# Kernel optimization log

Hardware: AMD Instinct MI355X
Metric: run time of the kernel (lower is better)

The kernel has to match this reference:

```python
import jax, jax.numpy as jnp
import numpy as np

B, T, C, H = 4, 2048, 1024, 16
D = C // H
NEG = -1e9


def setup_inputs() -> dict:
    key = jax.random.key(0)
    ks = jax.random.split(key, 4)
    x = jax.random.normal(ks[0], (B, T, C), dtype=jnp.float32)
    # additive causal mask: 0 on/below diagonal, -1e9 above
    causal = jnp.triu(jnp.full((T, T), NEG, dtype=jnp.float32), k=1)
    mask = causal[None, None, :, :]
    W_attn = jax.random.normal(ks[1], (C, 3 * C), dtype=jnp.float32) * (1.0 / np.sqrt(C))
    b_attn = jnp.zeros((3 * C,), dtype=jnp.float32)
    W_proj = jax.random.normal(ks[2], (C, C), dtype=jnp.float32) * (1.0 / np.sqrt(C))
    b_proj = jnp.zeros((C,), dtype=jnp.float32)
    return {"x": x, "mask": mask, "W_attn": W_attn, "b_attn": b_attn,
            "W_proj": W_proj, "b_proj": b_proj}


def reference(x, mask, W_attn, b_attn, W_proj, b_proj):
    b, t, c = x.shape
    qkv = x @ W_attn + b_attn                      # [b,t,3c]
    q, k, v = jnp.split(qkv, 3, axis=2)
    # [b,h,t,d]
    q = q.reshape(b, t, H, D).transpose(0, 2, 1, 3)
    k = k.reshape(b, t, H, D).transpose(0, 2, 1, 3)
    v = v.reshape(b, t, H, D).transpose(0, 2, 1, 3)
    att = jnp.einsum('bhqd,bhkd->bhqk', q, k) * (1.0 / np.sqrt(D))
    att = att + mask
    att = jax.nn.softmax(att, axis=-1)
    out = jnp.einsum('bhqk,bhkd->bhqd', att, v)    # [b,h,t,d]
    out = out.transpose(0, 2, 1, 3).reshape(b, t, c)
    out = out @ W_proj + b_proj
    return out, k, v
```

## Files before the change

kernel.cpp:

```cpp
#include <hip/hip_runtime.h>
#include <stdint.h>

typedef short  s16x8 __attribute__((ext_vector_type(8)));
typedef ushort u16x8 __attribute__((ext_vector_type(8)));
typedef float  f32x4 __attribute__((ext_vector_type(4)));

constexpr int BB = 4, TT = 2048, CC = 1024, HH = 16, DD = 64;
constexpr int MM = BB * TT;
constexpr int N_QKV = 3 * CC;
constexpr size_t KSEG = (size_t)MM * CC;
constexpr size_t VSEG = 2 * KSEG;

__device__ __forceinline__ ushort bf16_rne(float f) {
  uint32_t u = __builtin_bit_cast(uint32_t, f);
  u += 0x7fffu + ((u >> 16) & 1u);
  return (ushort)(u >> 16);
}
__device__ __forceinline__ float bf16_to_f32(ushort h) {
  uint32_t u = ((uint32_t)h) << 16;
  return __builtin_bit_cast(float, u);
}
__device__ __forceinline__ void split_hl(float f, ushort &hi, ushort &lo) {
  hi = bf16_rne(f);
  lo = bf16_rne(f - bf16_to_f32(hi));
}
__device__ __forceinline__ f32x4 mfma16(s16x8 a, s16x8 b, f32x4 c) {
  return __builtin_amdgcn_mfma_f32_16x16x32_bf16(a, b, c, 0, 0, 0);
}

__global__ void k_convert(const float* __restrict__ src, ushort* __restrict__ hi,
                          ushort* __restrict__ lo, int n8) {
  int i = blockIdx.x * blockDim.x + threadIdx.x;
  if (i >= n8) return;
  float4 a = ((const float4*)src)[2 * i];
  float4 b = ((const float4*)src)[2 * i + 1];
  float f[8] = {a.x, a.y, a.z, a.w, b.x, b.y, b.z, b.w};
  u16x8 h, l;
#pragma unroll
  for (int j = 0; j < 8; j++) { ushort hh, ll; split_hl(f[j], hh, ll); h[j] = hh; l[j] = ll; }
  *(u16x8*)(hi + 8 * (size_t)i) = h;
  *(u16x8*)(lo + 8 * (size_t)i) = l;
}

__global__ void k_transpose_split(const float* __restrict__ W, ushort* __restrict__ Th,
                                  ushort* __restrict__ Tl, int K, int N) {
  __shared__ float tile[32][33];
  int nt = blockIdx.x * 32, kt = blockIdx.y * 32;
  int tx = threadIdx.x, ty = threadIdx.y;
#pragma unroll
  for (int i = 0; i < 4; i++)
    tile[ty + i * 8][tx] = W[(size_t)(kt + ty + i * 8) * N + nt + tx];
  __syncthreads();
#pragma unroll
  for (int i = 0; i < 4; i++) {
    int nl = ty + i * 8;
    float f = tile[tx][nl];
    ushort h, l; split_hl(f, h, l);
    size_t o = (size_t)(nt + nl) * K + kt + tx;
    Th[o] = h; Tl[o] = l;
  }
}

template<int MODE>
__global__ __launch_bounds__(256) void k_gemm(
    const ushort* __restrict__ Ah, const ushort* __restrict__ Al,
    const ushort* __restrict__ Bth, const ushort* __restrict__ Btl,
    const float* __restrict__ bias, int K,
    float* __restrict__ outF, ushort* __restrict__ q_hi, ushort* __restrict__ q_lo,
    ushort* __restrict__ kh, ushort* __restrict__ kl,
    ushort* __restrict__ vth, ushort* __restrict__ vtl) {
  constexpr int LDK = 40;
  __shared__ ushort sAh[128 * LDK], sAl[128 * LDK], sBh[128 * LDK], sBl[128 * LDK];
  const int tid = threadIdx.x;
  const int wave = tid >> 6, lane = tid & 63;
  const int wr = wave >> 1, wc = wave & 1;
  const int lr = lane & 15, lg = lane >> 4;
  const int m0 = blockIdx.y * 128, n0 = blockIdx.x * 128;
  const int srow = tid >> 2;
  const int sk = (tid & 3) * 8;

  f32x4 acc[4][4] = {};

  for (int kt = 0; kt < K; kt += 32) {
#pragma unroll
    for (int p = 0; p < 2; p++) {
      int row = srow + p * 64;
      size_t ga = (size_t)(m0 + row) * K + kt + sk;
      size_t gb = (size_t)(n0 + row) * K + kt + sk;
      *(u16x8*)(sAh + row * LDK + sk) = *(const u16x8*)(Ah + ga);
      *(u16x8*)(sAl + row * LDK + sk) = *(const u16x8*)(Al + ga);
      *(u16x8*)(sBh + row * LDK + sk) = *(const u16x8*)(Bth + gb);
      *(u16x8*)(sBl + row * LDK + sk) = *(const u16x8*)(Btl + gb);
    }
    __syncthreads();
    s16x8 fah[4], fal[4], fbh[4], fbl[4];
#pragma unroll
    for (int i = 0; i < 4; i++) {
      fah[i] = *(const s16x8*)(sAh + (wr * 64 + i * 16 + lr) * LDK + lg * 8);
      fal[i] = *(const s16x8*)(sAl + (wr * 64 + i * 16 + lr) * LDK + lg * 8);
      fbh[i] = *(const s16x8*)(sBh + (wc * 64 + i * 16 + lr) * LDK + lg * 8);
      fbl[i] = *(const s16x8*)(sBl + (wc * 64 + i * 16 + lr) * LDK + lg * 8);
    }
#pragma unroll
    for (int mf = 0; mf < 4; mf++)
#pragma unroll
      for (int nf = 0; nf < 4; nf++) {
        acc[mf][nf] = mfma16(fah[mf], fbh[nf], acc[mf][nf]);
        acc[mf][nf] = mfma16(fah[mf], fbl[nf], acc[mf][nf]);
        acc[mf][nf] = mfma16(fal[mf], fbh[nf], acc[mf][nf]);
      }
    __syncthreads();
  }

#pragma unroll
  for (int mf = 0; mf < 4; mf++) {
#pragma unroll
    for (int nf = 0; nf < 4; nf++) {
      int n = n0 + wc * 64 + nf * 16 + lr;
      float bv = bias[n];
#pragma unroll
      for (int r = 0; r < 4; r++) {
        int m = m0 + wr * 64 + mf * 16 + lg * 4 + r;
        float v = acc[mf][nf][r] + bv;
        if constexpr (MODE == 0) {
          int b = m >> 11, t = m & 2047;
          int seg = n >> 10, nn = n & 1023;
          int h = nn >> 6, d = nn & 63;
          size_t idx = ((size_t)((b * 16 + h) * 2048 + t)) * 64 + d;
          if (seg == 0) {
            ushort hh, ll; split_hl(v * 0.125f, hh, ll);
            q_hi[idx] = hh; q_lo[idx] = ll;
          } else if (seg == 1) {
            outF[KSEG + idx] = v;
            ushort hh, ll; split_hl(v, hh, ll);
            kh[idx] = hh; kl[idx] = ll;
          } else {
            outF[VSEG + idx] = v;
            ushort hh, ll; split_hl(v, hh, ll);
            size_t vidx = ((size_t)((b * 16 + h) * 64 + d)) * 2048 + t;
            vth[vidx] = hh; vtl[vidx] = ll;
          }
        } else {
          outF[(size_t)m * CC + n] = v;
        }
      }
    }
  }
}

__global__ __launch_bounds__(256) void k_attn(
    const ushort* __restrict__ q_hi, const ushort* __restrict__ q_lo,
    const ushort* __restrict__ kh, const ushort* __restrict__ kl,
    const ushort* __restrict__ vth, const ushort* __restrict__ vtl,
    ushort* __restrict__ att_hi, ushort* __restrict__ att_lo) {
  constexpr int LD = 72;
  __shared__ ushort sK0[64 * LD], sK1[64 * LD];
  __shared__ ushort sV0[64 * LD], sV1[64 * LD];
  const int tid = threadIdx.x, wave = tid >> 6, lane = tid & 63;
  const int lr = lane & 15, lg = lane >> 4;
  const int qt = blockIdx.x, bh = blockIdx.y;
  const int qrow = qt * 64 + wave * 16;

  s16x8 fqh[2], fql[2];
  {
    size_t qb = ((size_t)bh * TT + qrow + lr) * 64;
#pragma unroll
    for (int ks = 0; ks < 2; ks++) {
      fqh[ks] = *(const s16x8*)(q_hi + qb + ks * 32 + lg * 8);
      fql[ks] = *(const s16x8*)(q_lo + qb + ks * 32 + lg * 8);
    }
  }
  float mrun[4], lrun[4];
#pragma unroll
  for (int r = 0; r < 4; r++) { mrun[r] = -INFINITY; lrun[r] = 0.f; }
  f32x4 oacc[4] = {};

  ushort* const Pb0 = sK0 + wave * 16 * LD;
  ushort* const Pb1 = sK1 + wave * 16 * LD;

  for (int kt = 0; kt <= qt; kt++) {
#pragma unroll
    for (int it = 0; it < 2; it++) {
      int vv = tid + it * 256;
      int row = vv >> 3, c8 = (vv & 7) * 8;
      size_t gk = ((size_t)bh * TT + kt * 64 + row) * 64 + c8;
      size_t gv = ((size_t)bh * 64 + row) * TT + kt * 64 + c8;
      *(u16x8*)(sK0 + row * LD + c8) = *(const u16x8*)(kh + gk);
      *(u16x8*)(sK1 + row * LD + c8) = *(const u16x8*)(kl + gk);
      *(u16x8*)(sV0 + row * LD + c8) = *(const u16x8*)(vth + gv);
      *(u16x8*)(sV1 + row * LD + c8) = *(const u16x8*)(vtl + gv);
    }
    __syncthreads();

    f32x4 sa[4];
#pragma unroll
    for (int nf = 0; nf < 4; nf++) {
      f32x4 a = {};
#pragma unroll
      for (int ks = 0; ks < 2; ks++) {
        s16x8 kbh = *(const s16x8*)(sK0 + (nf * 16 + lr) * LD + ks * 32 + lg * 8);
        s16x8 kbl = *(const s16x8*)(sK1 + (nf * 16 + lr) * LD + ks * 32 + lg * 8);
        a = mfma16(fqh[ks], kbh, a);
        a = mfma16(fqh[ks], kbl, a);
        a = mfma16(fql[ks], kbh, a);
      }
      sa[nf] = a;
    }
    if (kt == qt) {
#pragma unroll
      for (int nf = 0; nf < 4; nf++) {
        int colg = qt * 64 + nf * 16 + lr;
#pragma unroll
        for (int r = 0; r < 4; r++)
          if (colg > qrow + 4 * lg + r) sa[nf][r] = -1e9f;
      }
    }
    float fr[4];
#pragma unroll
    for (int r = 0; r < 4; r++) {
      float mx = fmaxf(fmaxf(sa[0][r], sa[1][r]), fmaxf(sa[2][r], sa[3][r]));
      mx = fmaxf(mx, __shfl_xor(mx, 1));
      mx = fmaxf(mx, __shfl_xor(mx, 2));
      mx = fmaxf(mx, __shfl_xor(mx, 4));
      mx = fmaxf(mx, __shfl_xor(mx, 8));
      float mnew = fmaxf(mrun[r], mx);
      fr[r] = __expf(mrun[r] - mnew);
      mrun[r] = mnew;
    }
    __syncthreads();
    float rs[4] = {0.f, 0.f, 0.f, 0.f};
#pragma unroll
    for (int nf = 0; nf < 4; nf++) {
#pragma unroll
      for (int r = 0; r < 4; r++) {
        float p = __expf(sa[nf][r] - mrun[r]);
        rs[r] += p;
        ushort h, l; split_hl(p, h, l);
        Pb0[(4 * lg + r) * LD + nf * 16 + lr] = h;
        Pb1[(4 * lg + r) * LD + nf * 16 + lr] = l;
      }
    }
#pragma unroll
    for (int r = 0; r < 4; r++) {
      float s = rs[r];
      s += __shfl_xor(s, 1); s += __shfl_xor(s, 2);
      s += __shfl_xor(s, 4); s += __shfl_xor(s, 8);
      lrun[r] = lrun[r] * fr[r] + s;
    }
#pragma unroll
    for (int df = 0; df < 4; df++)
#pragma unroll
      for (int r = 0; r < 4; r++) oacc[df][r] *= fr[r];

#pragma unroll
    for (int ks = 0; ks < 2; ks++) {
      s16x8 ph = *(const s16x8*)(Pb0 + lr * LD + ks * 32 + lg * 8);
      s16x8 pl = *(const s16x8*)(Pb1 + lr * LD + ks * 32 + lg * 8);
#pragma unroll
      for (int df = 0; df < 4; df++) {
        s16x8 bvh = *(const s16x8*)(sV0 + (df * 16 + lr) * LD + ks * 32 + lg * 8);
        s16x8 bvl = *(const s16x8*)(sV1 + (df * 16 + lr) * LD + ks * 32 + lg * 8);
        oacc[df] = mfma16(ph, bvh, oacc[df]);
        oacc[df] = mfma16(ph, bvl, oacc[df]);
        oacc[df] = mfma16(pl, bvh, oacc[df]);
      }
    }
    __syncthreads();
  }

  const int b = bh >> 4, h = bh & 15;
#pragma unroll
  for (int r = 0; r < 4; r++) {
    float inv = 1.0f / lrun[r];
    int t = qrow + 4 * lg + r;
#pragma unroll
    for (int df = 0; df < 4; df++) {
      float v = oacc[df][r] * inv;
      ushort hh, ll; split_hl(v, hh, ll);
      size_t idx = ((size_t)(b * TT + t)) * CC + h * 64 + df * 16 + lr;
      att_hi[idx] = hh; att_lo[idx] = ll;
    }
  }
}

extern "C" void kernel_launch(void* const* d_in, const int* in_sizes, int n_in,
                              void* d_out, int out_size, void* d_ws, size_t ws_size,
                              hipStream_t stream) {
  const float* x      = (const float*)d_in[0];
  const float* W_attn = (const float*)d_in[2];
  const float* b_attn = (const float*)d_in[3];
  const float* W_proj = (const float*)d_in[4];
  const float* b_proj = (const float*)d_in[5];
  float* out = (float*)d_out;

  char* w = (char*)d_ws;
  ushort* x_hi  = (ushort*)w; w += (size_t)MM * CC * 2;
  ushort* x_lo  = (ushort*)w; w += (size_t)MM * CC * 2;
  ushort* waT_h = (ushort*)w; w += (size_t)N_QKV * CC * 2;
  ushort* waT_l = (ushort*)w; w += (size_t)N_QKV * CC * 2;
  ushort* wpT_h = (ushort*)w; w += (size_t)CC * CC * 2;
  ushort* wpT_l = (ushort*)w; w += (size_t)CC * CC * 2;
  ushort* q_hi  = (ushort*)w; w += (size_t)MM * CC * 2;
  ushort* q_lo  = (ushort*)w; w += (size_t)MM * CC * 2;
  ushort* k_hi  = (ushort*)w; w += (size_t)MM * CC * 2;
  ushort* k_lo  = (ushort*)w; w += (size_t)MM * CC * 2;
  ushort* vT_hi = (ushort*)w; w += (size_t)MM * CC * 2;
  ushort* vT_lo = (ushort*)w; w += (size_t)MM * CC * 2;
  ushort* att_h = x_hi;
  ushort* att_l = x_lo;

  hipLaunchKernelGGL(k_convert, dim3((MM * CC / 8 + 255) / 256), dim3(256), 0, stream,
                     x, x_hi, x_lo, MM * CC / 8);
  hipLaunchKernelGGL(k_transpose_split, dim3(N_QKV / 32, CC / 32), dim3(32, 8), 0, stream,
                     W_attn, waT_h, waT_l, CC, N_QKV);
  hipLaunchKernelGGL(k_transpose_split, dim3(CC / 32, CC / 32), dim3(32, 8), 0, stream,
                     W_proj, wpT_h, wpT_l, CC, CC);
  hipLaunchKernelGGL((k_gemm<0>), dim3(N_QKV / 128, MM / 128), dim3(256), 0, stream,
                     x_hi, x_lo, waT_h, waT_l, b_attn, CC, out, q_hi, q_lo,
                     k_hi, k_lo, vT_hi, vT_lo);
  hipLaunchKernelGGL(k_attn, dim3(TT / 64, BB * HH), dim3(256), 0, stream,
                     q_hi, q_lo, k_hi, k_lo, vT_hi, vT_lo, att_h, att_l);
  hipLaunchKernelGGL((k_gemm<1>), dim3(CC / 128, MM / 128), dim3(256), 0, stream,
                     att_h, att_l, wpT_h, wpT_l, b_proj, CC, out,
                     nullptr, nullptr, nullptr, nullptr, nullptr, nullptr);
}
```

Before: 850.4 us.

## Pair causal query tiles per block, swizzle LDS, lazily rescale softmax

The attention kernel now processes two query tiles per block (tile px and 31-px), so every block does the same amount of causal work and each K/V tile load serves both queries. LDS padding is replaced by an XOR swizzle in both the GEMM and attention kernels, cutting shared memory while avoiding bank conflicts. The online softmax skips rescaling unless the running max grows by more than 8. P gets its own LDS buffer so one barrier per step can be removed, and launch bounds request 3 blocks per CU. Holding two query tiles of accumulators raises register pressure, and the lazy rescale trades some numeric headroom in the exponentials.

```diff
diff --git a/kernel.cpp b/kernel.cpp
--- a/kernel.cpp
+++ b/kernel.cpp
@@ -10,6 +10,9 @@
 constexpr int N_QKV = 3 * CC;
 constexpr size_t KSEG = (size_t)MM * CC;
 constexpr size_t VSEG = 2 * KSEG;
+
+#define SWZ64(row, uoff) ((row) * 64 + ((uoff) ^ (((row) & 7) << 3)))
+#define SWZ32(row, uoff) ((row) * 32 + ((uoff) ^ (((row) & 3) << 3)))
 
 __device__ __forceinline__ ushort bf16_rne(float f) {
   uint32_t u = __builtin_bit_cast(uint32_t, f);
@@ -69,8 +72,7 @@
     float* __restrict__ outF, ushort* __restrict__ q_hi, ushort* __restrict__ q_lo,
     ushort* __restrict__ kh, ushort* __restrict__ kl,
     ushort* __restrict__ vth, ushort* __restrict__ vtl) {
-  constexpr int LDK = 40;
-  __shared__ ushort sAh[128 * LDK], sAl[128 * LDK], sBh[128 * LDK], sBl[128 * LDK];
+  __shared__ ushort sAh[128 * 32], sAl[128 * 32], sBh[128 * 32], sBl[128 * 32];
   const int tid = threadIdx.x;
   const int wave = tid >> 6, lane = tid & 63;
   const int wr = wave >> 1, wc = wave & 1;
@@ -87,19 +89,21 @@
       int row = srow + p * 64;
       size_t ga = (size_t)(m0 + row) * K + kt + sk;
       size_t gb = (size_t)(n0 + row) * K + kt + sk;
-      *(u16x8*)(sAh + row * LDK + sk) = *(const u16x8*)(Ah + ga);
-      *(u16x8*)(sAl + row * LDK + sk) = *(const u16x8*)(Al + ga);
-      *(u16x8*)(sBh + row * LDK + sk) = *(const u16x8*)(Bth + gb);
-      *(u16x8*)(sBl + row * LDK + sk) = *(const u16x8*)(Btl + gb);
+      int d = SWZ32(row, sk);
+      *(u16x8*)(sAh + d) = *(const u16x8*)(Ah + ga);
+      *(u16x8*)(sAl + d) = *(const u16x8*)(Al + ga);
+      *(u16x8*)(sBh + d) = *(const u16x8*)(Bth + gb);
+      *(u16x8*)(sBl + d) = *(const u16x8*)(Btl + gb);
     }
     __syncthreads();
     s16x8 fah[4], fal[4], fbh[4], fbl[4];
 #pragma unroll
     for (int i = 0; i < 4; i++) {
-      fah[i] = *(const s16x8*)(sAh + (wr * 64 + i * 16 + lr) * LDK + lg * 8);
-      fal[i] = *(const s16x8*)(sAl + (wr * 64 + i * 16 + lr) * LDK + lg * 8);
-      fbh[i] = *(const s16x8*)(sBh + (wc * 64 + i * 16 + lr) * LDK + lg * 8);
-      fbl[i] = *(const s16x8*)(sBl + (wc * 64 + i * 16 + lr) * LDK + lg * 8);
+      int ra = wr * 64 + i * 16 + lr, rb = wc * 64 + i * 16 + lr;
+      fah[i] = *(const s16x8*)(sAh + SWZ32(ra, lg * 8));
+      fal[i] = *(const s16x8*)(sAl + SWZ32(ra, lg * 8));
+      fbh[i] = *(const s16x8*)(sBh + SWZ32(rb, lg * 8));
+      fbl[i] = *(const s16x8*)(sBl + SWZ32(rb, lg * 8));
     }
 #pragma unroll
     for (int mf = 0; mf < 4; mf++)
@@ -148,87 +152,91 @@
   }
 }
 
-__global__ __launch_bounds__(256) void k_attn(
+__global__ __launch_bounds__(256, 3) void k_attn(
     const ushort* __restrict__ q_hi, const ushort* __restrict__ q_lo,
     const ushort* __restrict__ kh, const ushort* __restrict__ kl,
     const ushort* __restrict__ vth, const ushort* __restrict__ vtl,
     ushort* __restrict__ att_hi, ushort* __restrict__ att_lo) {
-  constexpr int LD = 72;
-  __shared__ ushort sK0[64 * LD], sK1[64 * LD];
-  __shared__ ushort sV0[64 * LD], sV1[64 * LD];
+  __shared__ ushort sK0[64 * 64], sK1[64 * 64];
+  __shared__ ushort sV0[64 * 64], sV1[64 * 64];
+  __shared__ ushort sP0[4][16 * 64], sP1[4][16 * 64];
   const int tid = threadIdx.x, wave = tid >> 6, lane = tid & 63;
   const int lr = lane & 15, lg = lane >> 4;
-  const int qt = blockIdx.x, bh = blockIdx.y;
-  const int qrow = qt * 64 + wave * 16;
-
-  s16x8 fqh[2], fql[2];
+  const int px = blockIdx.x, bh = blockIdx.y;
+  const int qa = px, qb = 31 - px;
+  const int qrow_a = qa * 64 + wave * 16;
+  const int qrow_b = qb * 64 + wave * 16;
+
+  s16x8 fqah[2], fqal[2], fqbh[2], fqbl[2];
   {
-    size_t qb = ((size_t)bh * TT + qrow + lr) * 64;
+    size_t ba = ((size_t)bh * TT + qrow_a + lr) * 64;
+    size_t bb = ((size_t)bh * TT + qrow_b + lr) * 64;
 #pragma unroll
     for (int ks = 0; ks < 2; ks++) {
-      fqh[ks] = *(const s16x8*)(q_hi + qb + ks * 32 + lg * 8);
-      fql[ks] = *(const s16x8*)(q_lo + qb + ks * 32 + lg * 8);
-    }
-  }
-  float mrun[4], lrun[4];
-#pragma unroll
-  for (int r = 0; r < 4; r++) { mrun[r] = -INFINITY; lrun[r] = 0.f; }
-  f32x4 oacc[4] = {};
-
-  ushort* const Pb0 = sK0 + wave * 16 * LD;
-  ushort* const Pb1 = sK1 + wave * 16 * LD;
-
-  for (int kt = 0; kt <= qt; kt++) {
-#pragma unroll
-    for (int it = 0; it < 2; it++) {
-      int vv = tid + it * 256;
-      int row = vv >> 3, c8 = (vv & 7) * 8;
-      size_t gk = ((size_t)bh * TT + kt * 64 + row) * 64 + c8;
-      size_t gv = ((size_t)bh * 64 + row) * TT + kt * 64 + c8;
-      *(u16x8*)(sK0 + row * LD + c8) = *(const u16x8*)(kh + gk);
-      *(u16x8*)(sK1 + row * LD + c8) = *(const u16x8*)(kl + gk);
-      *(u16x8*)(sV0 + row * LD + c8) = *(const u16x8*)(vth + gv);
-      *(u16x8*)(sV1 + row * LD + c8) = *(const u16x8*)(vtl + gv);
-    }
-    __syncthreads();
-
+      fqah[ks] = *(const s16x8*)(q_hi + ba + ks * 32 + lg * 8);
+      fqal[ks] = *(const s16x8*)(q_lo + ba + ks * 32 + lg * 8);
+      fqbh[ks] = *(const s16x8*)(q_hi + bb + ks * 32 + lg * 8);
+      fqbl[ks] = *(const s16x8*)(q_lo + bb + ks * 32 + lg * 8);
+    }
+  }
+  float mra[4], lra[4], mrb[4], lrb[4];
+#pragma unroll
+  for (int r = 0; r < 4; r++) { mra[r] = -INFINITY; lra[r] = 0.f; mrb[r] = -INFINITY; lrb[r] = 0.f; }
+  f32x4 oa[4] = {}, ob[4] = {};
+
+  auto tile_step = [&](const s16x8* fqh, const s16x8* fql, float* mrun, float* lrun,
+                       f32x4* oacc, bool diag) {
     f32x4 sa[4];
 #pragma unroll
     for (int nf = 0; nf < 4; nf++) {
       f32x4 a = {};
 #pragma unroll
       for (int ks = 0; ks < 2; ks++) {
-        s16x8 kbh = *(const s16x8*)(sK0 + (nf * 16 + lr) * LD + ks * 32 + lg * 8);
-        s16x8 kbl = *(const s16x8*)(sK1 + (nf * 16 + lr) * LD + ks * 32 + lg * 8);
+        int d = SWZ64(nf * 16 + lr, ks * 32 + lg * 8);
+        s16x8 kbh = *(const s16x8*)(sK0 + d);
+        s16x8 kbl = *(const s16x8*)(sK1 + d);
         a = mfma16(fqh[ks], kbh, a);
         a = mfma16(fqh[ks], kbl, a);
         a = mfma16(fql[ks], kbh, a);
       }
       sa[nf] = a;
     }
-    if (kt == qt) {
+    if (diag) {
 #pragma unroll
       for (int nf = 0; nf < 4; nf++) {
-        int colg = qt * 64 + nf * 16 + lr;
+        int col = nf * 16 + lr;
 #pragma unroll
         for (int r = 0; r < 4; r++)
-          if (colg > qrow + 4 * lg + r) sa[nf][r] = -1e9f;
-      }
-    }
-    float fr[4];
+          if (col > wave * 16 + 4 * lg + r) sa[nf][r] = -1e9f;
+      }
+    }
+    float mx[4];
 #pragma unroll
     for (int r = 0; r < 4; r++) {
-      float mx = fmaxf(fmaxf(sa[0][r], sa[1][r]), fmaxf(sa[2][r], sa[3][r]));
-      mx = fmaxf(mx, __shfl_xor(mx, 1));
-      mx = fmaxf(mx, __shfl_xor(mx, 2));
-      mx = fmaxf(mx, __shfl_xor(mx, 4));
-      mx = fmaxf(mx, __shfl_xor(mx, 8));
-      float mnew = fmaxf(mrun[r], mx);
-      fr[r] = __expf(mrun[r] - mnew);
-      mrun[r] = mnew;
-    }
-    __syncthreads();
+      float m = fmaxf(fmaxf(sa[0][r], sa[1][r]), fmaxf(sa[2][r], sa[3][r]));
+      m = fmaxf(m, __shfl_xor(m, 1));
+      m = fmaxf(m, __shfl_xor(m, 2));
+      m = fmaxf(m, __shfl_xor(m, 4));
+      m = fmaxf(m, __shfl_xor(m, 8));
+      mx[r] = m;
+    }
+    int grow = 0;
+#pragma unroll
+    for (int r = 0; r < 4; r++) grow |= (mx[r] > mrun[r] + 8.0f);
+    if (__any(grow)) {
+#pragma unroll
+      for (int r = 0; r < 4; r++) {
+        float mnew = fmaxf(mrun[r], mx[r]);
+        float fr = __expf(mrun[r] - mnew);
+        mrun[r] = mnew;
+        lrun[r] *= fr;
+#pragma unroll
+        for (int df = 0; df < 4; df++) oacc[df][r] *= fr;
+      }
+    }
     float rs[4] = {0.f, 0.f, 0.f, 0.f};
+    ushort* Pb0 = sP0[wave];
+    ushort* Pb1 = sP1[wave];
 #pragma unroll
     for (int nf = 0; nf < 4; nf++) {
 #pragma unroll
@@ -236,8 +244,8 @@
         float p = __expf(sa[nf][r] - mrun[r]);
         rs[r] += p;
         ushort h, l; split_hl(p, h, l);
-        Pb0[(4 * lg + r) * LD + nf * 16 + lr] = h;
-        Pb1[(4 * lg + r) * LD + nf * 16 + lr] = l;
+        int d = SWZ64(4 * lg + r, nf * 16 + lr);
+        Pb0[d] = h; Pb1[d] = l;
       }
     }
 #pragma unroll
@@ -245,40 +253,57 @@
       float s = rs[r];
       s += __shfl_xor(s, 1); s += __shfl_xor(s, 2);
       s += __shfl_xor(s, 4); s += __shfl_xor(s, 8);
-      lrun[r] = lrun[r] * fr[r] + s;
-    }
-#pragma unroll
-    for (int df = 0; df < 4; df++)
-#pragma unroll
-      for (int r = 0; r < 4; r++) oacc[df][r] *= fr[r];
-
+      lrun[r] += s;
+    }
 #pragma unroll
     for (int ks = 0; ks < 2; ks++) {
-      s16x8 ph = *(const s16x8*)(Pb0 + lr * LD + ks * 32 + lg * 8);
-      s16x8 pl = *(const s16x8*)(Pb1 + lr * LD + ks * 32 + lg * 8);
+      int dp = SWZ64(lr, ks * 32 + lg * 8);
+      s16x8 ph = *(const s16x8*)(Pb0 + dp);
+      s16x8 pl = *(const s16x8*)(Pb1 + dp);
 #pragma unroll
       for (int df = 0; df < 4; df++) {
-        s16x8 bvh = *(const s16x8*)(sV0 + (df * 16 + lr) * LD + ks * 32 + lg * 8);
-        s16x8 bvl = *(const s16x8*)(sV1 + (df * 16 + lr) * LD + ks * 32 + lg * 8);
+        int dv = SWZ64(df * 16 + lr, ks * 32 + lg * 8);
+        s16x8 bvh = *(const s16x8*)(sV0 + dv);
+        s16x8 bvl = *(const s16x8*)(sV1 + dv);
         oacc[df] = mfma16(ph, bvh, oacc[df]);
         oacc[df] = mfma16(ph, bvl, oacc[df]);
         oacc[df] = mfma16(pl, bvh, oacc[df]);
       }
     }
+  };
+
+  for (int kt = 0; kt <= qb; kt++) {
+#pragma unroll
+    for (int it = 0; it < 2; it++) {
+      int vv = tid + it * 256;
+      int row = vv >> 3, cu = (vv & 7) * 8;
+      size_t gk = ((size_t)bh * TT + kt * 64 + row) * 64 + cu;
+      size_t gv = ((size_t)bh * 64 + row) * TT + kt * 64 + cu;
+      int d = SWZ64(row, cu);
+      *(u16x8*)(sK0 + d) = *(const u16x8*)(kh + gk);
+      *(u16x8*)(sK1 + d) = *(const u16x8*)(kl + gk);
+      *(u16x8*)(sV0 + d) = *(const u16x8*)(vth + gv);
+      *(u16x8*)(sV1 + d) = *(const u16x8*)(vtl + gv);
+    }
     __syncthreads();
+    if (kt <= qa) tile_step(fqah, fqal, mra, lra, oa, kt == qa);
+    tile_step(fqbh, fqbl, mrb, lrb, ob, kt == qb);
+    __syncthreads();
   }
 
   const int b = bh >> 4, h = bh & 15;
 #pragma unroll
   for (int r = 0; r < 4; r++) {
-    float inv = 1.0f / lrun[r];
-    int t = qrow + 4 * lg + r;
+    float inva = 1.0f / lra[r], invb = 1.0f / lrb[r];
+    int ta = qrow_a + 4 * lg + r, tb = qrow_b + 4 * lg + r;
 #pragma unroll
     for (int df = 0; df < 4; df++) {
-      float v = oacc[df][r] * inv;
-      ushort hh, ll; split_hl(v, hh, ll);
-      size_t idx = ((size_t)(b * TT + t)) * CC + h * 64 + df * 16 + lr;
-      att_hi[idx] = hh; att_lo[idx] = ll;
+      float va = oa[df][r] * inva, vb = ob[df][r] * invb;
+      ushort hh, ll;
+      size_t ia = ((size_t)(b * TT + ta)) * CC + h * 64 + df * 16 + lr;
+      size_t ib = ((size_t)(b * TT + tb)) * CC + h * 64 + df * 16 + lr;
+      split_hl(va, hh, ll); att_hi[ia] = hh; att_lo[ia] = ll;
+      split_hl(vb, hh, ll); att_hi[ib] = hh; att_lo[ib] = ll;
     }
   }
 }
@@ -318,7 +343,7 @@
   hipLaunchKernelGGL((k_gemm<0>), dim3(N_QKV / 128, MM / 128), dim3(256), 0, stream,
                      x_hi, x_lo, waT_h, waT_l, b_attn, CC, out, q_hi, q_lo,
                      k_hi, k_lo, vT_hi, vT_lo);
-  hipLaunchKernelGGL(k_attn, dim3(TT / 64, BB * HH), dim3(256), 0, stream,
+  hipLaunchKernelGGL(k_attn, dim3(16, BB * HH), dim3(256), 0, stream,
                      q_hi, q_lo, k_hi, k_lo, vT_hi, vT_lo, att_h, att_l);
   hipLaunchKernelGGL((k_gemm<1>), dim3(CC / 128, MM / 128), dim3(256), 0, stream,
                      att_h, att_l, wpT_h, wpT_l, b_proj, CC, out,
```

After: 738.9 us. 13.1% less time.
